# Kernel tuning notes

Hardware: AMD Instinct MI355X
Metric: run time of the kernel (lower is better)

The kernel has to match this reference:

```python
import jax, jax.numpy as jnp
import numpy as np

K = 4  # spline order (degree K-1)


def bspline_basis(x, t, k):
    """Evaluate the k nonzero B-spline basis functions of order k at x.

    x: [B, I] floats; t: [G+2k-1] clamped knot vector.
    Returns (idx [B,I,k] int32 basis indices, basis [B,I,k] values),
    using the de Boor / NURBS-book triangular recursion (vectorized over B,I;
    Python loops only over the small fixed order k).
    """
    m = t.shape[0]
    # interval index: t[i] <= x < t[i+1], clamped to valid span [k-1, m-k-1]
    i = jnp.clip(jnp.searchsorted(t, x, side='right') - 1, k - 1, m - k - 1)
    p = k - 1
    N = [jnp.ones_like(x)]
    left, right = [], []
    for j in range(1, p + 1):
        left.append(x - t[i + 1 - j])
        right.append(t[i + j] - x)
        saved = jnp.zeros_like(x)
        Nn = []
        for r in range(j):
            temp = N[r] / (right[r] + left[j - 1 - r])
            Nn.append(saved + right[r] * temp)
            saved = left[j - 1 - r] * temp
        Nn.append(saved)
        N = Nn
    idx = jnp.stack([i - p + j for j in range(k)], axis=-1)   # [B,I,k]
    basis = jnp.stack(N, axis=-1)                             # [B,I,k]
    return idx, basis


def setup_inputs() -> dict:
    key = jax.random.key(0)
    k1, k2 = jax.random.split(key)
    B, I, O, G, k = 2048, 128, 128, 64, K
    t0, t1 = -1.0, 1.0
    x = jax.random.uniform(k1, (B, I), jnp.float32, minval=t0, maxval=t1)
    # xavier_normal_ for fan_in=in_dim, fan_out=out_dim (per-slice heuristic)
    std = (2.0 / (I + O)) ** 0.5
    w = jax.random.normal(k2, (G + k, I, O), jnp.float32) * std
    t = jnp.concatenate([
        jnp.full((k - 1,), t0, jnp.float32),
        jnp.linspace(t0, t1, G + 1, dtype=jnp.float32),
        jnp.full((k - 1,), t1, jnp.float32),
    ])
    return {"x": x, "w": w, "t": t}


def reference(x, w, t):
    k = K
    B, I = x.shape
    O = w.shape[2]
    idx, basis = bspline_basis(x, t, k)                       # [B,I,k]
    # activation slot uses the last row of w (torch index -1)
    act_idx = jnp.full((B, I, 1), w.shape[0] - 1, idx.dtype)
    idx_full = jnp.concatenate([idx, act_idx], axis=-1)       # [B,I,k+1]
    y = jnp.concatenate([basis, jax.nn.silu(x)[..., None]], axis=-1)  # [B,I,k+1]
    wt = jnp.transpose(w, (1, 0, 2))                          # [I, G+k, O]
    w2 = wt[jnp.arange(I)[None, :, None], idx_full]           # [B,I,k+1,O] gather
    return jnp.einsum('bij,bijo->bo', y, w2)                  # [B,O]
```

## Files before the change

### kernel.cpp

```cpp
#include <hip/hip_runtime.h>
#include <math.h>

#define B_TOTAL 2048
#define I_DIM   128
#define O_DIM   128
#define GK      68
#define NKNOT   71
#define BT      64
#define RI      16
#define NR      (I_DIM / RI)
#define THREADS 512
#define SLICE_FLOATS (GK * O_DIM)
#define CHUNKS  (SLICE_FLOATS * 4 / 1024)
#define WS_NEED ((size_t)NR * B_TOTAL * O_DIM * 4)

template<bool USE_WS>
__global__ __launch_bounds__(THREADS)
void flashkan_main(const float* __restrict__ x,
                   const float* __restrict__ w,
                   const float* __restrict__ t,
                   float* __restrict__ dst) {
    __shared__ float wbuf[2][SLICE_FLOATS];
    __shared__ float coef[BT * RI * 6];
    __shared__ float t_sh[NKNOT];

    const int tid  = threadIdx.x;
    const int bid  = blockIdx.x;
    const int bt   = bid >> 3;
    const int r    = bid & 7;
    const int b0   = bt * BT;
    const int i0   = r * RI;
    const int wave = tid >> 6;
    const int lane = tid & 63;

    if (tid < NKNOT) t_sh[tid] = t[tid];
    __syncthreads();

    for (int p = tid; p < BT * RI; p += THREADS) {
        const int bl = p >> 4;
        const int ii = p & (RI - 1);
        const float xv = x[(size_t)(b0 + bl) * I_DIM + (i0 + ii)];

        int ik = 3 + (int)floorf((xv + 1.0f) * 32.0f);
        ik = min(max(ik, 3), 66);
        while (ik < 66 && xv >= t_sh[ik + 1]) ++ik;
        while (ik > 3 && xv < t_sh[ik]) --ik;

        float l0, l1, l2, r0, r1, r2;
        float N0 = 1.0f, N1, N2, N3;
        l0 = xv - t_sh[ik];
        r0 = t_sh[ik + 1] - xv;
        {
            float temp = N0 / (r0 + l0);
            N0 = r0 * temp;
            N1 = l0 * temp;
        }
        l1 = xv - t_sh[ik - 1];
        r1 = t_sh[ik + 2] - xv;
        {
            float saved = 0.0f, temp;
            temp = N0 / (r0 + l1);
            N0 = saved + r0 * temp;
            saved = l1 * temp;
            temp = N1 / (r1 + l0);
            N1 = saved + r1 * temp;
            N2 = l0 * temp;
        }
        l2 = xv - t_sh[ik - 2];
        r2 = t_sh[ik + 3] - xv;
        {
            float saved = 0.0f, temp;
            temp = N0 / (r0 + l2);
            N0 = saved + r0 * temp;
            saved = l2 * temp;
            temp = N1 / (r1 + l1);
            N1 = saved + r1 * temp;
            saved = l1 * temp;
            temp = N2 / (r2 + l0);
            N2 = saved + r2 * temp;
            N3 = l0 * temp;
        }
        const float silu = xv / (1.0f + expf(-xv));

        float* cp = &coef[p * 6];
        cp[0] = N0; cp[1] = N1; cp[2] = N2; cp[3] = N3;
        cp[4] = silu;
        cp[5] = __int_as_float(ik - 3);
    }

    auto stage = [&](int sel, int i_abs) {
        for (int c = wave; c < CHUNKS; c += 8) {
            const int f = c * 256 + lane * 4;
            const int g = f >> 7;
            const int o = f & (O_DIM - 1);
            const float* src = w + ((size_t)g * I_DIM + i_abs) * O_DIM + o;
            void* dstp = (void*)&wbuf[sel][c * 256];
            __builtin_amdgcn_global_load_lds(
                (const __attribute__((address_space(1))) void*)src,
                (__attribute__((address_space(3))) void*)dstp,
                16, 0, 0);
        }
    };

    stage(0, i0);
    __syncthreads();

    float2 acc[8];
    #pragma unroll
    for (int bl = 0; bl < 8; ++bl) acc[bl] = make_float2(0.0f, 0.0f);

    for (int ii = 0; ii < RI; ++ii) {
        if (ii + 1 < RI) stage((ii + 1) & 1, i0 + ii + 1);
        const float* buf = wbuf[ii & 1];

        #pragma unroll
        for (int bl = 0; bl < 8; ++bl) {
            const int blg = wave * 8 + bl;
            const float* cp = &coef[(blg * RI + ii) * 6];
            const float c0 = cp[0], c1 = cp[1], c2 = cp[2], c3 = cp[3], c4 = cp[4];
            const int   g0 = __float_as_int(cp[5]);

            const float2 v0 = ((const float2*)(buf + (size_t)(g0    ) * O_DIM))[lane];
            const float2 v1 = ((const float2*)(buf + (size_t)(g0 + 1) * O_DIM))[lane];
            const float2 v2 = ((const float2*)(buf + (size_t)(g0 + 2) * O_DIM))[lane];
            const float2 v3 = ((const float2*)(buf + (size_t)(g0 + 3) * O_DIM))[lane];
            const float2 v4 = ((const float2*)(buf + (size_t)(GK - 1) * O_DIM))[lane];

            acc[bl].x += c0 * v0.x + c1 * v1.x + c2 * v2.x + c3 * v3.x + c4 * v4.x;
            acc[bl].y += c0 * v0.y + c1 * v1.y + c2 * v2.y + c3 * v3.y + c4 * v4.y;
        }
        __syncthreads();
    }

    #pragma unroll
    for (int bl = 0; bl < 8; ++bl) {
        const int b = b0 + wave * 8 + bl;
        if (USE_WS) {
            float2* dp = (float2*)(dst + ((size_t)r * B_TOTAL + b) * O_DIM) + lane;
            *dp = acc[bl];
        } else {
            atomicAdd(&dst[(size_t)b * O_DIM + 2 * lane],     acc[bl].x);
            atomicAdd(&dst[(size_t)b * O_DIM + 2 * lane + 1], acc[bl].y);
        }
    }
}

__global__ __launch_bounds__(256)
void flashkan_reduce(const float* __restrict__ ws, float* __restrict__ out) {
    const int f = blockIdx.x * 256 + threadIdx.x;
    const float4* base = (const float4*)ws + f;
    float4 s = make_float4(0.0f, 0.0f, 0.0f, 0.0f);
    #pragma unroll
    for (int r2 = 0; r2 < NR; ++r2) {
        const float4 v = base[(size_t)r2 * (B_TOTAL * O_DIM / 4)];
        s.x += v.x; s.y += v.y; s.z += v.z; s.w += v.w;
    }
    ((float4*)out)[f] = s;
}

extern "C" void kernel_launch(void* const* d_in, const int* in_sizes, int n_in,
                              void* d_out, int out_size, void* d_ws, size_t ws_size,
                              hipStream_t stream) {
    const float* x = (const float*)d_in[0];
    const float* w = (const float*)d_in[1];
    const float* t = (const float*)d_in[2];
    float* out = (float*)d_out;

    dim3 grid(32 * NR);
    dim3 block(THREADS);

    if (ws_size >= WS_NEED) {
        float* ws = (float*)d_ws;
        flashkan_main<true><<<grid, block, 0, stream>>>(x, w, t, ws);
        flashkan_reduce<<<B_TOTAL * O_DIM / 4 / 256, 256, 0, stream>>>(ws, out);
    } else {
        hipMemsetAsync(out, 0, (size_t)out_size * sizeof(float), stream);
        flashkan_main<false><<<grid, block, 0, stream>>>(x, w, t, out);
    }
}
```

Measured before the change: 33.45 us.

## Halve I-split per block, hold spline coefficients in registers via readlane

The input dimension is split into 16 ranges of 8 instead of 8 ranges of 16, doubling the grid to 512 blocks for better occupancy. A launch-bounds hint targets 4 blocks per CU. Each lane now computes one (batch, input) coefficient set and keeps it in registers, and the inner loop broadcasts it with readlane instead of storing to and reading from an LDS coef array. The double-buffer loop is unrolled by two with fixed buffer indices and the silu row load is hoisted. The cost is a workspace that is twice as large and a reduction over 16 partials instead of 8.

```diff
diff --git a/kernel.cpp b/kernel.cpp
--- a/kernel.cpp
+++ b/kernel.cpp
@@ -7,27 +7,30 @@
 #define GK      68
 #define NKNOT   71
 #define BT      64
-#define RI      16
+#define RI      8
 #define NR      (I_DIM / RI)
 #define THREADS 512
 #define SLICE_FLOATS (GK * O_DIM)
-#define CHUNKS  (SLICE_FLOATS * 4 / 1024)
+#define CHUNKS  (SLICE_FLOATS / 256)
 #define WS_NEED ((size_t)NR * B_TOTAL * O_DIM * 4)
 
+__device__ __forceinline__ float rdlanef(float v, int l) {
+    return __int_as_float(__builtin_amdgcn_readlane(__float_as_int(v), l));
+}
+
 template<bool USE_WS>
-__global__ __launch_bounds__(THREADS)
+__global__ __launch_bounds__(THREADS, 4)
 void flashkan_main(const float* __restrict__ x,
                    const float* __restrict__ w,
                    const float* __restrict__ t,
                    float* __restrict__ dst) {
     __shared__ float wbuf[2][SLICE_FLOATS];
-    __shared__ float coef[BT * RI * 6];
     __shared__ float t_sh[NKNOT];
 
     const int tid  = threadIdx.x;
     const int bid  = blockIdx.x;
-    const int bt   = bid >> 3;
-    const int r    = bid & 7;
+    const int bt   = bid >> 4;
+    const int r    = bid & 15;
     const int b0   = bt * BT;
     const int i0   = r * RI;
     const int wave = tid >> 6;
@@ -36,10 +39,12 @@
     if (tid < NKNOT) t_sh[tid] = t[tid];
     __syncthreads();
 
-    for (int p = tid; p < BT * RI; p += THREADS) {
-        const int bl = p >> 4;
-        const int ii = p & (RI - 1);
-        const float xv = x[(size_t)(b0 + bl) * I_DIM + (i0 + ii)];
+    float cf0, cf1, cf2, cf3, cf4;
+    int   cg;
+    {
+        const int bl = lane >> 3;
+        const int ii = lane & 7;
+        const float xv = x[(size_t)(b0 + wave * 8 + bl) * I_DIM + (i0 + ii)];
 
         int ik = 3 + (int)floorf((xv + 1.0f) * 32.0f);
         ik = min(max(ik, 3), 66);
@@ -80,12 +85,9 @@
             N2 = saved + r2 * temp;
             N3 = l0 * temp;
         }
-        const float silu = xv / (1.0f + expf(-xv));
-
-        float* cp = &coef[p * 6];
-        cp[0] = N0; cp[1] = N1; cp[2] = N2; cp[3] = N3;
-        cp[4] = silu;
-        cp[5] = __int_as_float(ik - 3);
+        cf0 = N0; cf1 = N1; cf2 = N2; cf3 = N3;
+        cf4 = xv / (1.0f + expf(-xv));
+        cg  = ik - 3;
     }
 
     auto stage = [&](int sel, int i_abs) {
@@ -102,33 +104,42 @@
         }
     };
 
-    stage(0, i0);
-    __syncthreads();
-
     float2 acc[8];
     #pragma unroll
     for (int bl = 0; bl < 8; ++bl) acc[bl] = make_float2(0.0f, 0.0f);
 
-    for (int ii = 0; ii < RI; ++ii) {
-        if (ii + 1 < RI) stage((ii + 1) & 1, i0 + ii + 1);
-        const float* buf = wbuf[ii & 1];
-
+    auto compute = [&](int ii, const float* buf) {
+        const float2 v4 = ((const float2*)(buf + 67 * O_DIM))[lane];
         #pragma unroll
         for (int bl = 0; bl < 8; ++bl) {
-            const int blg = wave * 8 + bl;
-            const float* cp = &coef[(blg * RI + ii) * 6];
-            const float c0 = cp[0], c1 = cp[1], c2 = cp[2], c3 = cp[3], c4 = cp[4];
-            const int   g0 = __float_as_int(cp[5]);
+            const int src = (bl << 3) | ii;
+            const float c0 = rdlanef(cf0, src);
+            const float c1 = rdlanef(cf1, src);
+            const float c2 = rdlanef(cf2, src);
+            const float c3 = rdlanef(cf3, src);
+            const float c4 = rdlanef(cf4, src);
+            const int   g0 = __builtin_amdgcn_readlane(cg, src);
 
-            const float2 v0 = ((const float2*)(buf + (size_t)(g0    ) * O_DIM))[lane];
-            const float2 v1 = ((const float2*)(buf + (size_t)(g0 + 1) * O_DIM))[lane];
-            const float2 v2 = ((const float2*)(buf + (size_t)(g0 + 2) * O_DIM))[lane];
-            const float2 v3 = ((const float2*)(buf + (size_t)(g0 + 3) * O_DIM))[lane];
-            const float2 v4 = ((const float2*)(buf + (size_t)(GK - 1) * O_DIM))[lane];
+            const float2* rp = (const float2*)(buf + (size_t)g0 * O_DIM) + lane;
+            const float2 v0 = rp[0];
+            const float2 v1 = rp[64];
+            const float2 v2 = rp[128];
+            const float2 v3 = rp[192];
 
             acc[bl].x += c0 * v0.x + c1 * v1.x + c2 * v2.x + c3 * v3.x + c4 * v4.x;
             acc[bl].y += c0 * v0.y + c1 * v1.y + c2 * v2.y + c3 * v3.y + c4 * v4.y;
         }
+    };
+
+    stage(0, i0);
+    __syncthreads();
+
+    for (int iib = 0; iib < RI; iib += 2) {
+        stage(1, i0 + iib + 1);
+        compute(iib, wbuf[0]);
+        __syncthreads();
+        if (iib + 2 < RI) stage(0, i0 + iib + 2);
+        compute(iib + 1, wbuf[1]);
         __syncthreads();
     }
 
```

Measured after the change: 31.95 us. -4.5%, faster.
